# Kernel optimization log

Measured on AMD Instinct MI355X. Metric: run time of the kernel, lower is better.

## Reference

```python
import jax, jax.numpy as jnp
import numpy as np

SR = 44100.0
MIN_RATE = 0.1
MAX_RATE = 5.0
K = 4        # number of cascaded all-pass stages
HIDDEN = 16  # MLP hidden width
N_SAMPLES = 524288


def setup_inputs() -> dict:
    key = jax.random.key(0)
    ks = jax.random.split(key, 6)
    x = jax.random.normal(ks[0], (2, N_SAMPLES), dtype=jnp.float32)
    lfo_rate_0to1 = jax.random.uniform(ks[1], (1,), dtype=jnp.float32)
    lfo_stereo_phase_offset_0to1 = jax.random.uniform(ks[2], (1,), dtype=jnp.float32)
    # learned params of the pretrained grey-box phaser model
    W1 = 0.1 * jax.random.normal(ks[3], (1, HIDDEN), dtype=jnp.float32)
    b1 = jnp.zeros((HIDDEN,), dtype=jnp.float32)
    W2 = 0.1 * jax.random.normal(ks[4], (HIDDEN, 1), dtype=jnp.float32)
    b2 = jnp.zeros((1,), dtype=jnp.float32)
    lfo_amp = jnp.array(1.0, dtype=jnp.float32)
    bias = jnp.array(0.3, dtype=jnp.float32)
    depth = jnp.array(0.9, dtype=jnp.float32)
    g1 = jnp.array(0.2, dtype=jnp.float32)
    prev_phase = jnp.array(0.0, dtype=jnp.float32)
    return {"x": x, "lfo_rate_0to1": lfo_rate_0to1,
            "lfo_stereo_phase_offset_0to1": lfo_stereo_phase_offset_0to1,
            "W1": W1, "b1": b1, "W2": W2, "b2": b2,
            "lfo_amp": lfo_amp, "bias": bias, "depth": depth,
            "g1": g1, "prev_phase": prev_phase}


def reference(x, lfo_rate_0to1, lfo_stereo_phase_offset_0to1,
              W1, b1, W2, b2, lfo_amp, bias, depth, g1, prev_phase):
    n = x.shape[-1]
    two_pi = 2.0 * jnp.pi
    rate = lfo_rate_0to1[0] * (MAX_RATE - MIN_RATE) + MIN_RATE
    phase_off = lfo_stereo_phase_offset_0to1[0] * two_pi
    # cumsum of a constant -> closed form (arange starts at 1, matching cumsum)
    arg_l = (two_pi * rate / SR) * jnp.arange(1, n + 1, dtype=x.dtype) + prev_phase
    arg = jnp.stack([arg_l, arg_l + phase_off], axis=0)          # (2, N)
    lfo = (lfo_amp * jnp.cos(arg))[..., None]                    # (2, N, 1)
    h = jnp.tanh(lfo @ W1 + b1)                                  # (2, N, H)
    m = (h @ W2 + b2)[..., 0]                                    # (2, N)
    d = bias + depth * 0.5 * (1.0 + m)
    td = jnp.tan(d)
    p = jnp.tanh((1.0 - td) / (1.0 + td))                        # (2, N) TV all-pass coeff

    def step(carry, inp):
        xprev, yprev = carry    # each (K,)
        xn, pn = inp
        u = xn + g1 * yprev[K - 1]   # feedback from last stage
        nx, ny = [], []
        for k in range(K):           # fixed small cascade, unrolled
            y = pn * u + xprev[k] - pn * yprev[k]
            nx.append(u)
            ny.append(y)
            u = y
        out = 0.5 * (xn + u)
        return (jnp.stack(nx), jnp.stack(ny)), out

    def run_channel(xc, pc):
        init = (jnp.zeros((K,), xc.dtype), jnp.zeros((K,), xc.dtype))
        _, out = jax.lax.scan(step, init, (xc, pc))
        return out

    return jax.vmap(run_channel)(x, p)  # (2, N)
```

## Files before the change

kernel.cpp:

```cpp
#include <hip/hip_runtime.h>
#include <math.h>

#define NSAMP 524288
#define CHUNK 16
#define WGT 256
#define NWGC 128
#define TOTWG 256
#define HIDDEN 16
#define NTAB 256

typedef float f32x2 __attribute__((ext_vector_type(2)));

__device__ __forceinline__ float fast_tanh(float x) {
    float e = __expf(2.0f * x);
    return (e - 1.0f) / (e + 1.0f);
}

__device__ __forceinline__ void compose6(const f32x2* A, const f32x2* B,
                                         f32x2* O) {
#pragma unroll
    for (int r = 0; r < 5; ++r) {
        f32x2 acc0 = {0.0f, 0.0f};
        f32x2 acc1 = {0.0f, 0.0f};
        f32x2 acc2 = {0.0f, A[r*3 + 2][1]};
#pragma unroll
        for (int k = 0; k < 5; ++k) {
            float a = A[r*3 + k/2][k%2];
            f32x2 as = {a, a};
            acc0 += as * B[k*3 + 0];
            acc1 += as * B[k*3 + 1];
            acc2 += as * B[k*3 + 2];
        }
        O[r*3 + 0] = acc0; O[r*3 + 1] = acc1; O[r*3 + 2] = acc2;
    }
}

__device__ __forceinline__ void set_identity6(f32x2* T) {
#pragma unroll
    for (int q = 0; q < 15; ++q) { f32x2 z = {0.0f, 0.0f}; T[q] = z; }
#pragma unroll
    for (int r = 0; r < 5; ++r) T[(7*r)/2][(7*r)%2] = 1.0f;
}

__device__ __forceinline__ float ld_agent(const float* p) {
    return __hip_atomic_load(p, __ATOMIC_RELAXED, __HIP_MEMORY_SCOPE_AGENT);
}
__device__ __forceinline__ void st_agent(float* p, float v) {
    __hip_atomic_store(p, v, __ATOMIC_RELAXED, __HIP_MEMORY_SCOPE_AGENT);
}
__device__ __forceinline__ unsigned ldu_agent(const unsigned* p) {
    return __hip_atomic_load(p, __ATOMIC_RELAXED, __HIP_MEMORY_SCOPE_AGENT);
}
__device__ __forceinline__ void stu_agent(unsigned* p, unsigned v) {
    __hip_atomic_store(p, v, __ATOMIC_RELAXED, __HIP_MEMORY_SCOPE_AGENT);
}

__device__ __forceinline__ void wave_incl_scan6(f32x2* T, int l) {
#pragma unroll
    for (int off = 1; off < 64; off <<= 1) {
        f32x2 p[15];
#pragma unroll
        for (int q = 0; q < 15; ++q) {
            p[q][0] = __shfl_up(T[q][0], (unsigned)off);
            p[q][1] = __shfl_up(T[q][1], (unsigned)off);
        }
        if (l >= off) {
            f32x2 n[15];
            compose6(T, p, n);
#pragma unroll
            for (int q = 0; q < 15; ++q) T[q] = n[q];
        }
    }
}

__device__ __forceinline__ void wave_prefix6(const f32x2 wAp[][16], int w,
                                             f32x2* P) {
    if (w == 0) { set_identity6(P); return; }
#pragma unroll
    for (int q = 0; q < 15; ++q) P[q] = wAp[0][q];
    for (int j = 1; j < w; ++j) {
        f32x2 Wm[15], n[15];
#pragma unroll
        for (int q = 0; q < 15; ++q) Wm[q] = wAp[j][q];
        compose6(Wm, P, n);
#pragma unroll
        for (int q = 0; q < 15; ++q) P[q] = n[q];
    }
}

__global__ void __launch_bounds__(WGT, 1) k_fused(
    const float* __restrict__ X,
    const float* __restrict__ rate01,
    const float* __restrict__ phoff01,
    const float* __restrict__ W1,
    const float* __restrict__ b1,
    const float* __restrict__ W2,
    const float* __restrict__ b2,
    const float* __restrict__ amp,
    const float* __restrict__ bias_,
    const float* __restrict__ depth_,
    const float* __restrict__ g1p,
    const float* __restrict__ prevph,
    float* __restrict__ OUT,
    float* __restrict__ RECT,
    float* __restrict__ EST,
    unsigned int* __restrict__ FLG,
    unsigned int* __restrict__ FLG2)
{
    __shared__ float Tp[NTAB];
    __shared__ f32x2 wA[4][16];
    __shared__ float sES[8];

    const int t   = threadIdx.x;
    const int vid = blockIdx.x;
    const int c   = vid >> 7;
    const int wc  = vid & (NWGC - 1);
    const int w   = t >> 6;
    const int l   = t & 63;

    const int gblk = wc * WGT + t;
    const long base = (long)c * NSAMP + (long)gblk * CHUNK;

    float xv[CHUNK];
    {
        const float4* Xv = (const float4*)(X + base);
#pragma unroll
        for (int q = 0; q < CHUNK / 4; ++q) {
            float4 a = Xv[q];
            xv[q*4+0]=a.x; xv[q*4+1]=a.y; xv[q*4+2]=a.z; xv[q*4+3]=a.w;
        }
    }

    const float two_pi = 6.28318530717958647692f;
    const float rate   = fmaf(rate01[0], 4.9f, 0.1f);
    const float w0rev  = rate / 44100.0f;
    const float dscale = depth_[0] * 0.5f;
    const float g1     = g1p[0];

    {
        float lfo = amp[0] * __cosf((float)t * (two_pi / (float)NTAB));
        float m = b2[0];
#pragma unroll
        for (int jj = 0; jj < HIDDEN; ++jj) {
            float h = fast_tanh(fmaf(lfo, W1[jj], b1[jj]));
            m = fmaf(h, W2[jj], m);
        }
        float dd = fmaf(dscale, 1.0f + m, bias_[0]);
        float td = __tanf(dd);
        Tp[t] = fast_tanh((1.0f - td) / (1.0f + td));
    }
    __syncthreads();

    const float phrev = prevph[0] * (1.0f / two_pi) + (c ? phoff01[0] : 0.0f);

    float pv[CHUNK];
#pragma unroll
    for (int k = 0; k < CHUNK; ++k) {
        float ph = fmaf(w0rev, (float)(gblk * CHUNK + k + 1), phrev);
        float u = (ph - floorf(ph)) * (float)NTAB;
        int i0 = ((int)u) & (NTAB - 1);
        float f = u - floorf(u);
        int i1 = (i0 + 1) & (NTAB - 1);
        float t0 = Tp[i0];
        pv[k] = fmaf(f, Tp[i1] - t0, t0);
    }

    f32x2 v2[3][5];
#pragma unroll
    for (int p = 0; p < 3; ++p)
#pragma unroll
        for (int r = 0; r < 5; ++r) {
            f32x2 e; e[0] = (2*p == r) ? 1.0f : 0.0f;
            e[1] = (2*p + 1 == r) ? 1.0f : 0.0f;
            v2[p][r] = e;
        }

    {
        const f32x2 g1s = {g1, g1};
#pragma unroll
        for (int k = 0; k < CHUNK; ++k) {
            const f32x2 pp2 = {pv[k], pv[k]};
#pragma unroll
            for (int p = 0; p < 3; ++p) {
                f32x2 xin2 = {0.0f, (p == 2) ? xv[k] : 0.0f};
                f32x2 u0 = g1s * v2[p][4] + xin2;
                f32x2 y0 = pp2 * (u0 - v2[p][1]) + v2[p][0];
                f32x2 y1 = pp2 * (y0 - v2[p][2]) + v2[p][1];
                f32x2 y2 = pp2 * (y1 - v2[p][3]) + v2[p][2];
                f32x2 y3 = pp2 * (y2 - v2[p][4]) + v2[p][3];
                v2[p][0] = u0; v2[p][1] = y0; v2[p][2] = y1;
                v2[p][3] = y2; v2[p][4] = y3;
            }
        }
    }

    f32x2 T[15];
#pragma unroll
    for (int r = 0; r < 5; ++r) {
        T[r*3 + 0] = v2[0][r];
        T[r*3 + 1] = v2[1][r];
        T[r*3 + 2] = v2[2][r];
    }

    wave_incl_scan6(T, l);
    if (l == 63) {
#pragma unroll
        for (int q = 0; q < 15; ++q) wA[w][q] = T[q];
    }
    __syncthreads();
    f32x2 P[15];
    wave_prefix6(wA, w, P);

    if (t == WGT - 1) {
        f32x2 Tot[15];
        compose6(T, P, Tot);
#pragma unroll
        for (int k = 0; k < 30; ++k)
            st_agent(&RECT[k*TOTWG + vid], Tot[k/2][k%2]);
    }
    __syncthreads();
    if (t == 0) {
        asm volatile("" ::: "memory");
        stu_agent(&FLG[vid], 1u);
    }

    if (wc == 0) {
        f32x2 aT[15];
        if (t < NWGC) {
            const unsigned int* fp = &FLG[c * NWGC + t];
            while (ldu_agent(fp) != 1u) { __builtin_amdgcn_s_sleep(1); }
            asm volatile("" ::: "memory");
#pragma unroll
            for (int k = 0; k < 30; ++k)
                aT[k/2][k%2] = ld_agent(&RECT[k*TOTWG + c*NWGC + t]);
            stu_agent((unsigned int*)&FLG[c * NWGC + t], 0u);
        } else {
            set_identity6(aT);
        }

        wave_incl_scan6(aT, l);
        if (l == 63) {
#pragma unroll
            for (int q = 0; q < 15; ++q) wA[w][q] = aT[q];
        }
        __syncthreads();
        f32x2 aP[15];
        wave_prefix6(wA, w, aP);
        float aPd[5];
#pragma unroll
        for (int j = 0; j < 5; ++j) aPd[j] = aP[(j*6+5)/2][(j*6+5)%2];

        float es[5];
#pragma unroll
        for (int r = 0; r < 5; ++r) {
            float acc = __shfl_up(aT[r*3 + 2][1], 1u);
#pragma unroll
            for (int j = 0; j < 5; ++j)
                acc = fmaf(__shfl_up(aT[r*3 + j/2][j%2], 1u), aPd[j], acc);
            es[r] = (l == 0) ? aPd[r] : acc;
        }
        if (t < NWGC) {
#pragma unroll
            for (int r = 0; r < 5; ++r)
                st_agent(&EST[r*TOTWG + c*NWGC + t], es[r]);
        }
        __syncthreads();
        asm volatile("" ::: "memory");
        if (t < NWGC)
            stu_agent(&FLG2[c * NWGC + t], 1u);
    }

    if (t == 0) {
        if (wc != 0) {
            unsigned int* fp = &FLG2[vid];
            while (ldu_agent(fp) != 1u) { }
            asm volatile("" ::: "memory");
#pragma unroll
            for (int r = 0; r < 5; ++r)
                sES[r] = ld_agent(&EST[r*TOTWG + vid]);
            stu_agent(fp, 0u);
        } else {
#pragma unroll
            for (int r = 0; r < 5; ++r) sES[r] = 0.0f;
        }
    }
    __syncthreads();
    float sw[5];
#pragma unroll
    for (int r = 0; r < 5; ++r) sw[r] = sES[r];

    float s1[5];
    if (w == 0) {
#pragma unroll
        for (int r = 0; r < 5; ++r) s1[r] = sw[r];
    } else {
#pragma unroll
        for (int r = 0; r < 5; ++r) {
            float acc = P[r*3 + 2][1];
#pragma unroll
            for (int j = 0; j < 5; ++j)
                acc = fmaf(P[r*3 + j/2][j%2], sw[j], acc);
            s1[r] = acc;
        }
    }
    float s0, s1r, s2, s3, s4;
    {
        float s[5];
#pragma unroll
        for (int r = 0; r < 5; ++r) {
            float acc = __shfl_up(T[r*3 + 2][1], 1u);
#pragma unroll
            for (int j = 0; j < 5; ++j)
                acc = fmaf(__shfl_up(T[r*3 + j/2][j%2], 1u), s1[j], acc);
            s[r] = (l == 0) ? s1[r] : acc;
        }
        s0 = s[0]; s1r = s[1]; s2 = s[2]; s3 = s[3]; s4 = s[4];
    }

    {
        float4* Ov = (float4*)(OUT + base);
#pragma unroll
        for (int q = 0; q < CHUNK / 4; ++q) {
            float oa[4];
#pragma unroll
            for (int ii = 0; ii < 4; ++ii) {
                float pp = pv[q*4 + ii], xx = xv[q*4 + ii];
                float u0 = fmaf(g1, s4, xx);
                float y0 = fmaf(pp, u0 - s1r, s0);
                float y1 = fmaf(pp, y0 - s2, s1r);
                float y2 = fmaf(pp, y1 - s3, s2);
                float y3 = fmaf(pp, y2 - s4, s3);
                s0 = u0; s1r = y0; s2 = y1; s3 = y2; s4 = y3;
                oa[ii] = 0.5f * (xx + y3);
            }
            float4 o; o.x = oa[0]; o.y = oa[1]; o.z = oa[2]; o.w = oa[3];
            Ov[q] = o;
        }
    }
}

extern "C" void kernel_launch(void* const* d_in, const int* in_sizes, int n_in,
                              void* d_out, int out_size, void* d_ws, size_t ws_size,
                              hipStream_t stream) {
    const float* x     = (const float*)d_in[0];
    const float* rate  = (const float*)d_in[1];
    const float* phoff = (const float*)d_in[2];
    const float* W1    = (const float*)d_in[3];
    const float* b1    = (const float*)d_in[4];
    const float* W2    = (const float*)d_in[5];
    const float* b2    = (const float*)d_in[6];
    const float* amp   = (const float*)d_in[7];
    const float* bias_ = (const float*)d_in[8];
    const float* depth = (const float*)d_in[9];
    const float* g1    = (const float*)d_in[10];
    const float* pph   = (const float*)d_in[11];
    float* out = (float*)d_out;

    float* RECT = (float*)d_ws;
    float* EST  = RECT + 30L * TOTWG;
    unsigned int* FLG  = (unsigned int*)(EST + 5L * TOTWG);
    unsigned int* FLG2 = FLG + TOTWG;

    k_fused<<<dim3(TOTWG), dim3(WGT), 0, stream>>>(
        x, rate, phoff, W1, b1, W2, b2, amp, bias_, depth, g1, pph,
        out, RECT, EST, FLG, FLG2);
}
```

Before: 21.74 us.

## Replace two-phase cross-workgroup scan with per-block redundant prefix via flag matrix

Instead of having workgroup 0 of each channel collect all block aggregates, scan them, and publish per-block start states via a second flag round, every workgroup now waits on its own predecessors' aggregates and composes them locally. A per-pair flag matrix replaces the two flag arrays, removing one global serialization round and the dependency on a single coordinator block. This trades extra redundant loads and scan work per block (up to 128 aggregates each) and more flag traffic for lower latency on the critical path.

```diff
diff --git a/kernel.cpp b/kernel.cpp
--- a/kernel.cpp
+++ b/kernel.cpp
@@ -103,9 +103,7 @@
     const float* __restrict__ prevph,
     float* __restrict__ OUT,
     float* __restrict__ RECT,
-    float* __restrict__ EST,
-    unsigned int* __restrict__ FLG,
-    unsigned int* __restrict__ FLG2)
+    unsigned int* __restrict__ FLGM)
 {
     __shared__ float Tp[NTAB];
     __shared__ f32x2 wA[4][16];
@@ -219,72 +217,42 @@
             st_agent(&RECT[k*TOTWG + vid], Tot[k/2][k%2]);
     }
     __syncthreads();
-    if (t == 0) {
+    if (t < NWGC) {
         asm volatile("" ::: "memory");
-        stu_agent(&FLG[vid], 1u);
-    }
-
-    if (wc == 0) {
-        f32x2 aT[15];
-        if (t < NWGC) {
-            const unsigned int* fp = &FLG[c * NWGC + t];
-            while (ldu_agent(fp) != 1u) { __builtin_amdgcn_s_sleep(1); }
-            asm volatile("" ::: "memory");
-#pragma unroll
-            for (int k = 0; k < 30; ++k)
-                aT[k/2][k%2] = ld_agent(&RECT[k*TOTWG + c*NWGC + t]);
-            stu_agent((unsigned int*)&FLG[c * NWGC + t], 0u);
-        } else {
-            set_identity6(aT);
-        }
-
+        stu_agent(&FLGM[(c * NWGC + t) * NWGC + wc], 1u);
+    }
+
+    f32x2 aT[15];
+    if (t < wc) {
+        unsigned int* fp = &FLGM[(c * NWGC + wc) * NWGC + t];
+        while (ldu_agent(fp) != 1u) { __builtin_amdgcn_s_sleep(1); }
+        asm volatile("" ::: "memory");
+#pragma unroll
+        for (int k = 0; k < 30; ++k)
+            aT[k/2][k%2] = ld_agent(&RECT[k*TOTWG + c*NWGC + t]);
+        stu_agent(fp, 0u);
+    } else {
+        set_identity6(aT);
+    }
+
+    if (w < 2) {
         wave_incl_scan6(aT, l);
         if (l == 63) {
 #pragma unroll
             for (int q = 0; q < 15; ++q) wA[w][q] = aT[q];
         }
-        __syncthreads();
-        f32x2 aP[15];
-        wave_prefix6(wA, w, aP);
-        float aPd[5];
-#pragma unroll
-        for (int j = 0; j < 5; ++j) aPd[j] = aP[(j*6+5)/2][(j*6+5)%2];
-
-        float es[5];
-#pragma unroll
-        for (int r = 0; r < 5; ++r) {
-            float acc = __shfl_up(aT[r*3 + 2][1], 1u);
-#pragma unroll
-            for (int j = 0; j < 5; ++j)
-                acc = fmaf(__shfl_up(aT[r*3 + j/2][j%2], 1u), aPd[j], acc);
-            es[r] = (l == 0) ? aPd[r] : acc;
-        }
-        if (t < NWGC) {
-#pragma unroll
-            for (int r = 0; r < 5; ++r)
-                st_agent(&EST[r*TOTWG + c*NWGC + t], es[r]);
-        }
-        __syncthreads();
-        asm volatile("" ::: "memory");
-        if (t < NWGC)
-            stu_agent(&FLG2[c * NWGC + t], 1u);
-    }
-
+    }
+    __syncthreads();
     if (t == 0) {
-        if (wc != 0) {
-            unsigned int* fp = &FLG2[vid];
-            while (ldu_agent(fp) != 1u) { }
-            asm volatile("" ::: "memory");
-#pragma unroll
-            for (int r = 0; r < 5; ++r)
-                sES[r] = ld_agent(&EST[r*TOTWG + vid]);
-            stu_agent(fp, 0u);
-        } else {
-#pragma unroll
-            for (int r = 0; r < 5; ++r) sES[r] = 0.0f;
-        }
-    }
-    __syncthreads();
+        f32x2 W0[15], W1v[15], Tot[15];
+#pragma unroll
+        for (int q = 0; q < 15; ++q) { W0[q] = wA[0][q]; W1v[q] = wA[1][q]; }
+        compose6(W1v, W0, Tot);
+#pragma unroll
+        for (int r = 0; r < 5; ++r) sES[r] = Tot[r*3 + 2][1];
+    }
+    __syncthreads();
+
     float sw[5];
 #pragma unroll
     for (int r = 0; r < 5; ++r) sw[r] = sES[r];
@@ -357,11 +325,9 @@
     float* out = (float*)d_out;
 
     float* RECT = (float*)d_ws;
-    float* EST  = RECT + 30L * TOTWG;
-    unsigned int* FLG  = (unsigned int*)(EST + 5L * TOTWG);
-    unsigned int* FLG2 = FLG + TOTWG;
+    unsigned int* FLGM = (unsigned int*)(RECT + 30L * TOTWG);
 
     k_fused<<<dim3(TOTWG), dim3(WGT), 0, stream>>>(
         x, rate, phoff, W1, b1, W2, b2, amp, bias_, depth, g1, pph,
-        out, RECT, EST, FLG, FLG2);
-}
+        out, RECT, FLGM);
+}
```

Result: faster. 19.61 us (-9.8%).
